# Performance work log

Hardware: AMD Instinct MI355X
Metric: run time of the kernel (lower is better)

The kernel has to match this reference:

```python
import jax, jax.numpy as jnp
import numpy as np

HID = 64      # RNN hidden size (fixed in source)
K = 3         # B-spline order (pykan default)
NUM = 5       # grid intervals (pykan default)
DIMS = [64, 16, 1]  # layer_nums_small_nobi


def make_grid(in_dim):
    # uniform grid on [-1,1] extended by K knots each side -> NUM+2K+1 = 12 knots
    h = 2.0 / NUM
    g = jnp.arange(-K, NUM + K + 1, dtype=jnp.float32) * h - 1.0
    return jnp.broadcast_to(g, (in_dim, g.shape[0]))


def bspline_basis(x, grid):
    # x: (b, in), grid: (in, G) -> basis (b, in, G-K-1) via Cox-de Boor
    xe = x[..., None]
    B = ((xe >= grid[:, :-1]) & (xe < grid[:, 1:])).astype(x.dtype)
    for d in range(1, K + 1):
        left = (xe - grid[:, :-(d + 1)]) / (grid[:, d:-1] - grid[:, :-(d + 1)]) * B[..., :-1]
        right = (grid[:, d + 1:] - xe) / (grid[:, d + 1:] - grid[:, 1:-d]) * B[..., 1:]
        B = left + right
    return B  # (b, in, NUM+K)


def kan_layer(x, grid, coef, sb, sp):
    # coef: (in, out, NUM+K); sb, sp: (in, out)
    bas = bspline_basis(x, grid)                      # (b, in, NUM+K)
    spl = jnp.einsum('bik,iok->bio', bas, coef)       # per-edge spline value
    return jnp.einsum('bi,io->bo', jax.nn.silu(x), sb) + jnp.einsum('bio,io->bo', spl, sp)


def rnn_layer(x, w_ih, w_hh, b_ih, b_hh, return_seq):
    # x: (b, t, f), tanh RNN, h0 = 0
    h0 = jnp.zeros((x.shape[0], HID), x.dtype)
    def step(h, xt):
        h = jnp.tanh(xt @ w_ih.T + h @ w_hh.T + b_ih + b_hh)
        return h, (h if return_seq else 0.0)
    hT, ys = jax.lax.scan(step, h0, jnp.swapaxes(x, 0, 1))
    return jnp.swapaxes(ys, 0, 1) if return_seq else hT


def setup_inputs() -> dict:
    key = jax.random.key(0)
    ks = jax.random.split(key, 16)
    Bsz, T, F = 2048, 256, 64
    s = 1.0 / np.sqrt(HID)
    inp = {'x': jax.random.normal(ks[0], (Bsz, T, F), jnp.float32)}
    inp['w_ih0'] = jax.random.uniform(ks[1], (HID, F), jnp.float32, -s, s)
    inp['w_hh0'] = jax.random.uniform(ks[2], (HID, HID), jnp.float32, -s, s)
    inp['b_ih0'] = jax.random.uniform(ks[3], (HID,), jnp.float32, -s, s)
    inp['b_hh0'] = jax.random.uniform(ks[4], (HID,), jnp.float32, -s, s)
    inp['w_ih1'] = jax.random.uniform(ks[5], (HID, HID), jnp.float32, -s, s)
    inp['w_hh1'] = jax.random.uniform(ks[6], (HID, HID), jnp.float32, -s, s)
    inp['b_ih1'] = jax.random.uniform(ks[7], (HID,), jnp.float32, -s, s)
    inp['b_hh1'] = jax.random.uniform(ks[8], (HID,), jnp.float32, -s, s)
    kk = 9
    for i, (di, do) in enumerate(zip(DIMS[:-1], DIMS[1:])):
        inp[f'grid{i}'] = make_grid(di)
        inp[f'coef{i}'] = 0.1 * jax.random.normal(ks[kk], (di, do, NUM + K), jnp.float32)
        inp[f'sb{i}'] = (1.0 / np.sqrt(di)) * jnp.ones((di, do), jnp.float32) + 0.05 * jax.random.normal(ks[kk + 1], (di, do), jnp.float32)
        inp[f'sp{i}'] = jnp.ones((di, do), jnp.float32)
        kk += 2
    return inp


def reference(x, w_ih0, w_hh0, b_ih0, b_hh0, w_ih1, w_hh1, b_ih1, b_hh1,
              grid0, coef0, sb0, sp0, grid1, coef1, sb1, sp1):
    h1 = rnn_layer(x, w_ih0, w_hh0, b_ih0, b_hh0, return_seq=True)   # (b,t,64)
    out = rnn_layer(h1, w_ih1, w_hh1, b_ih1, b_hh1, return_seq=False)  # last step only
    out = kan_layer(out, grid0, coef0, sb0, sp0)   # (b,16)
    out = kan_layer(out, grid1, coef1, sb1, sp1)   # (b,1)
    return jnp.squeeze(jax.nn.sigmoid(out), 1)     # (b,)
```

## Files before the change

### kernel.cpp

```cpp
#include <hip/hip_runtime.h>
#include <cstdint>
#include <cstddef>

typedef __attribute__((ext_vector_type(8))) __bf16 bf16x8;
typedef __attribute__((ext_vector_type(4))) float f32x4;

#define MFMA16(a, b, c) __builtin_amdgcn_mfma_f32_16x16x32_bf16((a), (b), (c), 0, 0, 0)

__device__ __forceinline__ float fast_tanh(float z) {
    float e = __expf(2.0f * z);
    return 1.0f - 2.0f * __builtin_amdgcn_rcpf(e + 1.0f);
}
__device__ __forceinline__ float fast_sigmoid(float z) {
    return __builtin_amdgcn_rcpf(1.0f + __expf(-z));
}

__device__ __forceinline__ f32x4 gload4(const float* p) {
    return *(const __attribute__((address_space(1))) f32x4*)p;
}

__device__ __forceinline__ unsigned pk2(float a, float b) {
    union { __bf16 h[2]; unsigned u; } p;
    p.h[0] = (__bf16)a;
    p.h[1] = (__bf16)b;
    return p.u;
}

__device__ __forceinline__ bf16x8 cvt8(f32x4 a, f32x4 b) {
    bf16x8 f;
    f[0] = (__bf16)a[0]; f[1] = (__bf16)a[1]; f[2] = (__bf16)a[2]; f[3] = (__bf16)a[3];
    f[4] = (__bf16)b[0]; f[5] = (__bf16)b[1]; f[6] = (__bf16)b[2]; f[7] = (__bf16)b[3];
    return f;
}

__device__ __forceinline__ bf16x8 ldwfrag(const float* __restrict__ W, int row, int k0) {
    const f32x4 a = *(const f32x4*)(W + row * 64 + k0);
    const f32x4 b = *(const f32x4*)(W + row * 64 + k0 + 4);
    return cvt8(a, b);
}

__device__ __forceinline__ void bspl8(float x, const float* kn, float* B) {
    float b[11];
#pragma unroll
    for (int m = 0; m < 11; ++m)
        b[m] = (x >= kn[m] && x < kn[m + 1]) ? 1.0f : 0.0f;
#pragma unroll
    for (int d = 1; d <= 3; ++d) {
#pragma unroll
        for (int m = 0; m + d < 11; ++m) {
            float lf = (x - kn[m]) / (kn[m + d] - kn[m]) * b[m];
            float rt = (kn[m + d + 1] - x) / (kn[m + d + 1] - kn[m + 1]) * b[m + 1];
            b[m] = lf + rt;
        }
    }
#pragma unroll
    for (int m = 0; m < 8; ++m) B[m] = b[m];
}

__global__ __launch_bounds__(256, 1) void rnn_kan_v6(
    const float* __restrict__ x,
    const float* __restrict__ wih0, const float* __restrict__ whh0,
    const float* __restrict__ bih0, const float* __restrict__ bhh0,
    const float* __restrict__ wih1, const float* __restrict__ whh1,
    const float* __restrict__ bih1, const float* __restrict__ bhh1,
    const float* __restrict__ grid0, const float* __restrict__ coef0,
    const float* __restrict__ sb0, const float* __restrict__ sp0,
    const float* __restrict__ grid1, const float* __restrict__ coef1,
    const float* __restrict__ sb1, const float* __restrict__ sp1,
    float* __restrict__ out)
{
    __shared__ __align__(16) unsigned char s_h[2][4096];
    __shared__ __align__(16) float s_hf[16][68];
    __shared__ __align__(16) float s_bas[1024][12];
    __shared__ __align__(16) float s_e[16][17];

    const int tid  = threadIdx.x;
    const int wv   = tid >> 6;
    const int lane = tid & 63;
    const int sc   = lane & 15;
    const int gr   = lane >> 4;
    const int s0   = blockIdx.x << 4;

    const int wrow = 16 * wv + sc;
    const int kofs = 8 * gr;
    bf16x8 fWih0[2], fWhh0[2], fWih1[2], fWhh1[2];
#pragma unroll
    for (int kt = 0; kt < 2; ++kt) {
        fWih0[kt] = ldwfrag(wih0, wrow, 32 * kt + kofs);
        fWhh0[kt] = ldwfrag(whh0, wrow, 32 * kt + kofs);
        fWih1[kt] = ldwfrag(wih1, wrow, 32 * kt + kofs);
        fWhh1[kt] = ldwfrag(whh1, wrow, 32 * kt + kofs);
    }
    f32x4 b0v, b1v, zv;
#pragma unroll
    for (int i = 0; i < 4; ++i) {
        const int h = 16 * wv + 4 * gr + i;
        b0v[i] = bih0[h] + bhh0[h];
        b1v[i] = bih1[h] + bhh1[h];
        zv[i] = 0.0f;
    }

    const unsigned swz  = (unsigned)(sc & 7) << 4;
    const unsigned offW  = sc * 128 + (((unsigned)(32 * wv + 8 * gr)) ^ swz);
    const unsigned offR0 = sc * 128 + (((unsigned)(16 * gr)) ^ swz);
    const unsigned offR1 = sc * 128 + (((unsigned)(64 + 16 * gr)) ^ swz);

    const float* xb = x + (size_t)(s0 + sc) * 16384 + kofs;

    f32x4 q0 = gload4(xb),        q1 = gload4(xb + 4);
    f32x4 q2 = gload4(xb + 32),   q3 = gload4(xb + 36);
    f32x4 p0 = gload4(xb + 64),   p1 = gload4(xb + 68);
    f32x4 p2 = gload4(xb + 96),   p3 = gload4(xb + 100);
    f32x4 r0[3], r1[3], r2[3], r3[3];
#pragma unroll
    for (int j = 0; j < 3; ++j) {
        const float* pj = xb + (size_t)(2 + j) * 64;
        r0[j] = gload4(pj);      r1[j] = gload4(pj + 4);
        r2[j] = gload4(pj + 32); r3[j] = gload4(pj + 36);
    }

    f32x4 xz = MFMA16(fWih0[0], cvt8(q0, q1), b0v);
    xz = MFMA16(fWih0[1], cvt8(q2, q3), xz);

    {
        float v[4];
#pragma unroll
        for (int i = 0; i < 4; ++i) v[i] = fast_tanh(xz[i]);
        uint2 pw; pw.x = pk2(v[0], v[1]); pw.y = pk2(v[2], v[3]);
        *(uint2*)((char*)(&s_h[0][0]) + offW) = pw;
    }
    *(uint2*)((char*)(&s_h[0][0]) + 2048 + offW) = make_uint2(0u, 0u);

    xz = MFMA16(fWih0[0], cvt8(p0, p1), b0v);
    xz = MFMA16(fWih0[1], cvt8(p2, p3), xz);

    asm volatile("s_waitcnt lgkmcnt(0)" ::: "memory");
    __builtin_amdgcn_s_barrier();
    asm volatile("" ::: "memory");

    bf16x8 h1f0 = *(const bf16x8*)((const char*)(&s_h[0][0]) + offR0);
    bf16x8 h1f1 = *(const bf16x8*)((const char*)(&s_h[0][0]) + offR1);
    f32x4 h2z = b1v;

#pragma unroll 3
    for (int t = 1; t < 256; ++t) {
        const int slot = (t - 1) % 3;
        char* hb = (char*)(&s_h[0][0]) + ((t & 1) << 12);

        f32x4 z1a = MFMA16(fWhh0[0], h1f0, xz);
        f32x4 z1b = MFMA16(fWhh0[1], h1f1, zv);
        f32x4 z2a = MFMA16(fWih1[0], h1f0, h2z);
        f32x4 z2b = MFMA16(fWih1[1], h1f1, zv);

        f32x4 z1 = z1a + z1b;
        float v1[4];
#pragma unroll
        for (int i = 0; i < 4; ++i) v1[i] = fast_tanh(z1[i]);
        uint2 pw1; pw1.x = pk2(v1[0], v1[1]); pw1.y = pk2(v1[2], v1[3]);
        *(uint2*)(hb + offW) = pw1;

        f32x4 z2 = z2a + z2b;
        float v2[4];
#pragma unroll
        for (int i = 0; i < 4; ++i) v2[i] = fast_tanh(z2[i]);
        uint2 pw2; pw2.x = pk2(v2[0], v2[1]); pw2.y = pk2(v2[2], v2[3]);
        *(uint2*)(hb + 2048 + offW) = pw2;

        xz = MFMA16(fWih0[0], cvt8(r0[slot], r1[slot]), b0v);
        xz = MFMA16(fWih0[1], cvt8(r2[slot], r3[slot]), xz);
        {
            const float* pn = xb + (size_t)((t + 4 > 255) ? 255 : t + 4) * 64;
            r0[slot] = gload4(pn);      r1[slot] = gload4(pn + 4);
            r2[slot] = gload4(pn + 32); r3[slot] = gload4(pn + 36);
        }

        asm volatile("s_waitcnt lgkmcnt(0)" ::: "memory");
        __builtin_amdgcn_s_barrier();
        asm volatile("" ::: "memory");

        h1f0 = *(const bf16x8*)(hb + offR0);
        h1f1 = *(const bf16x8*)(hb + offR1);
        bf16x8 h2f0 = *(const bf16x8*)(hb + 2048 + offR0);
        bf16x8 h2f1 = *(const bf16x8*)(hb + 2048 + offR1);

        h2z = MFMA16(fWhh1[0], h2f0, b1v);
        h2z = MFMA16(fWhh1[1], h2f1, h2z);
    }

    {
        f32x4 z2a = MFMA16(fWih1[0], h1f0, h2z);
        f32x4 z2b = MFMA16(fWih1[1], h1f1, zv);
        f32x4 z2 = z2a + z2b;
        f32x4 hv;
#pragma unroll
        for (int i = 0; i < 4; ++i) hv[i] = fast_tanh(z2[i]);
        *(f32x4*)(&s_hf[sc][16 * wv + 4 * gr]) = hv;
    }
    __syncthreads();

    float kn0[12], kn1[12];
#pragma unroll
    for (int m = 0; m < 12; ++m) { kn0[m] = grid0[m]; kn1[m] = grid1[m]; }

    for (int q = tid; q < 1024; q += 256) {
        const int i = q >> 4, s = q & 15;
        const float v = s_hf[s][i];
        float B[8];
        bspl8(v, kn0, B);
        *(float4*)(&s_bas[q][0]) = make_float4(B[0], B[1], B[2], B[3]);
        *(float4*)(&s_bas[q][4]) = make_float4(B[4], B[5], B[6], B[7]);
        s_bas[q][8] = v * fast_sigmoid(v);
    }
    __syncthreads();

    {
        const int s = tid >> 4, o = tid & 15;
        float acc = 0.0f;
        for (int i = 0; i < 64; ++i) {
            const int q = (i << 4) + s;
            const float4 B0 = *(const float4*)(&s_bas[q][0]);
            const float4 B1 = *(const float4*)(&s_bas[q][4]);
            const float sil = s_bas[q][8];
            const float* cp = coef0 + i * 128 + o * 8;
            const float4 c0 = *(const float4*)cp;
            const float4 c1 = *(const float4*)(cp + 4);
            const float spl = B0.x * c0.x + B0.y * c0.y + B0.z * c0.z + B0.w * c0.w +
                              B1.x * c1.x + B1.y * c1.y + B1.z * c1.z + B1.w * c1.w;
            acc += sil * sb0[(i << 4) + o] + sp0[(i << 4) + o] * spl;
        }
        float B[8];
        bspl8(acc, kn1, B);
        const float* cp = coef1 + o * 8;
        float spl = 0.0f;
#pragma unroll
        for (int k = 0; k < 8; ++k) spl += B[k] * cp[k];
        s_e[s][o] = (acc * fast_sigmoid(acc)) * sb1[o] + sp1[o] * spl;
    }
    __syncthreads();

    if (tid < 16) {
        float sum = 0.0f;
#pragma unroll
        for (int o = 0; o < 16; ++o) sum += s_e[tid][o];
        out[s0 + tid] = fast_sigmoid(sum);
    }
}

extern "C" void kernel_launch(void* const* d_in, const int* in_sizes, int n_in,
                              void* d_out, int out_size, void* d_ws, size_t ws_size,
                              hipStream_t stream) {
    (void)n_in; (void)out_size; (void)d_ws; (void)ws_size;
    const int B = in_sizes[0] / (256 * 64);
    const int grid = B / 16;
    rnn_kan_v6<<<dim3(grid), dim3(256), 0, stream>>>(
        (const float*)d_in[0],
        (const float*)d_in[1], (const float*)d_in[2], (const float*)d_in[3], (const float*)d_in[4],
        (const float*)d_in[5], (const float*)d_in[6], (const float*)d_in[7], (const float*)d_in[8],
        (const float*)d_in[9], (const float*)d_in[10], (const float*)d_in[11], (const float*)d_in[12],
        (const float*)d_in[13], (const float*)d_in[14], (const float*)d_in[15], (const float*)d_in[16],
        (float*)d_out);
}
```

Before: 146.5 us.

## Split RNN recurrence into three warp-specialized roles pipelined across timesteps

The block grows from 4 to 12 waves, split into three roles. One role computes the input projection for layer 0 and the input-to-hidden product for layer 1, one runs the layer-0 recurrence, and one runs the layer-1 recurrence one step behind, all handing data through double-buffered shared memory. This shortens the serial dependency chain per barrier and spreads the MFMA and tanh work over more waves. In exchange the loop runs two extra steps and needs more shared memory, and the larger block can lower occupancy and make each barrier more expensive.

Result: slower. 358.5 us (+144.7%).

```diff
diff --git a/kernel.cpp b/kernel.cpp
--- a/kernel.cpp
+++ b/kernel.cpp
@@ -57,7 +57,7 @@
     for (int m = 0; m < 8; ++m) B[m] = b[m];
 }
 
-__global__ __launch_bounds__(256, 1) void rnn_kan_v6(
+__global__ __launch_bounds__(768) void rnn_kan_v8(
     const float* __restrict__ x,
     const float* __restrict__ wih0, const float* __restrict__ whh0,
     const float* __restrict__ bih0, const float* __restrict__ bhh0,
@@ -69,7 +69,10 @@
     const float* __restrict__ sb1, const float* __restrict__ sp1,
     float* __restrict__ out)
 {
-    __shared__ __align__(16) unsigned char s_h[2][4096];
+    __shared__ __align__(16) float s_xz[2][16 * 64];
+    __shared__ __align__(16) float s_p2[2][16 * 64];
+    __shared__ __align__(16) unsigned char s_h1[2][2048];
+    __shared__ __align__(16) unsigned char s_h2[2][2048];
     __shared__ __align__(16) float s_hf[16][68];
     __shared__ __align__(16) float s_bas[1024][12];
     __shared__ __align__(16) float s_e[16][17];
@@ -79,130 +82,117 @@
     const int lane = tid & 63;
     const int sc   = lane & 15;
     const int gr   = lane >> 4;
+    const int role = wv >> 2;
+    const int rt   = wv & 3;
     const int s0   = blockIdx.x << 4;
 
-    const int wrow = 16 * wv + sc;
-    const int kofs = 8 * gr;
-    bf16x8 fWih0[2], fWhh0[2], fWih1[2], fWhh1[2];
-#pragma unroll
-    for (int kt = 0; kt < 2; ++kt) {
-        fWih0[kt] = ldwfrag(wih0, wrow, 32 * kt + kofs);
-        fWhh0[kt] = ldwfrag(whh0, wrow, 32 * kt + kofs);
-        fWih1[kt] = ldwfrag(wih1, wrow, 32 * kt + kofs);
-        fWhh1[kt] = ldwfrag(whh1, wrow, 32 * kt + kofs);
-    }
-    f32x4 b0v, b1v, zv;
-#pragma unroll
-    for (int i = 0; i < 4; ++i) {
-        const int h = 16 * wv + 4 * gr + i;
-        b0v[i] = bih0[h] + bhh0[h];
-        b1v[i] = bih1[h] + bhh1[h];
-        zv[i] = 0.0f;
-    }
-
     const unsigned swz  = (unsigned)(sc & 7) << 4;
-    const unsigned offW  = sc * 128 + (((unsigned)(32 * wv + 8 * gr)) ^ swz);
+    const unsigned offW  = sc * 128 + (((unsigned)(32 * rt + 8 * gr)) ^ swz);
     const unsigned offR0 = sc * 128 + (((unsigned)(16 * gr)) ^ swz);
     const unsigned offR1 = sc * 128 + (((unsigned)(64 + 16 * gr)) ^ swz);
-
-    const float* xb = x + (size_t)(s0 + sc) * 16384 + kofs;
-
-    f32x4 q0 = gload4(xb),        q1 = gload4(xb + 4);
-    f32x4 q2 = gload4(xb + 32),   q3 = gload4(xb + 36);
-    f32x4 p0 = gload4(xb + 64),   p1 = gload4(xb + 68);
-    f32x4 p2 = gload4(xb + 96),   p3 = gload4(xb + 100);
-    f32x4 r0[3], r1[3], r2[3], r3[3];
-#pragma unroll
-    for (int j = 0; j < 3; ++j) {
-        const float* pj = xb + (size_t)(2 + j) * 64;
-        r0[j] = gload4(pj);      r1[j] = gload4(pj + 4);
-        r2[j] = gload4(pj + 32); r3[j] = gload4(pj + 36);
-    }
-
-    f32x4 xz = MFMA16(fWih0[0], cvt8(q0, q1), b0v);
-    xz = MFMA16(fWih0[1], cvt8(q2, q3), xz);
-
-    {
-        float v[4];
-#pragma unroll
-        for (int i = 0; i < 4; ++i) v[i] = fast_tanh(xz[i]);
-        uint2 pw; pw.x = pk2(v[0], v[1]); pw.y = pk2(v[2], v[3]);
-        *(uint2*)((char*)(&s_h[0][0]) + offW) = pw;
-    }
-    *(uint2*)((char*)(&s_h[0][0]) + 2048 + offW) = make_uint2(0u, 0u);
-
-    xz = MFMA16(fWih0[0], cvt8(p0, p1), b0v);
-    xz = MFMA16(fWih0[1], cvt8(p2, p3), xz);
-
-    asm volatile("s_waitcnt lgkmcnt(0)" ::: "memory");
-    __builtin_amdgcn_s_barrier();
-    asm volatile("" ::: "memory");
-
-    bf16x8 h1f0 = *(const bf16x8*)((const char*)(&s_h[0][0]) + offR0);
-    bf16x8 h1f1 = *(const bf16x8*)((const char*)(&s_h[0][0]) + offR1);
-    f32x4 h2z = b1v;
-
-#pragma unroll 3
-    for (int t = 1; t < 256; ++t) {
-        const int slot = (t - 1) % 3;
-        char* hb = (char*)(&s_h[0][0]) + ((t & 1) << 12);
-
-        f32x4 z1a = MFMA16(fWhh0[0], h1f0, xz);
-        f32x4 z1b = MFMA16(fWhh0[1], h1f1, zv);
-        f32x4 z2a = MFMA16(fWih1[0], h1f0, h2z);
-        f32x4 z2b = MFMA16(fWih1[1], h1f1, zv);
-
-        f32x4 z1 = z1a + z1b;
-        float v1[4];
-#pragma unroll
-        for (int i = 0; i < 4; ++i) v1[i] = fast_tanh(z1[i]);
-        uint2 pw1; pw1.x = pk2(v1[0], v1[1]); pw1.y = pk2(v1[2], v1[3]);
-        *(uint2*)(hb + offW) = pw1;
-
-        f32x4 z2 = z2a + z2b;
-        float v2[4];
-#pragma unroll
-        for (int i = 0; i < 4; ++i) v2[i] = fast_tanh(z2[i]);
-        uint2 pw2; pw2.x = pk2(v2[0], v2[1]); pw2.y = pk2(v2[2], v2[3]);
-        *(uint2*)(hb + 2048 + offW) = pw2;
-
-        xz = MFMA16(fWih0[0], cvt8(r0[slot], r1[slot]), b0v);
-        xz = MFMA16(fWih0[1], cvt8(r2[slot], r3[slot]), xz);
-        {
-            const float* pn = xb + (size_t)((t + 4 > 255) ? 255 : t + 4) * 64;
-            r0[slot] = gload4(pn);      r1[slot] = gload4(pn + 4);
-            r2[slot] = gload4(pn + 32); r3[slot] = gload4(pn + 36);
-        }
-
+    const unsigned offX  = sc * 256 + (((unsigned)(64 * rt + 16 * gr)) ^ swz);
+
+    for (int i = tid; i < 512; i += 768) ((unsigned*)&s_h1[1][0])[i] = 0u;
+    for (int i = tid; i < 1024; i += 768) ((unsigned*)&s_h2[0][0])[i] = 0u;
+
+    bf16x8 fA0, fA1, fB0, fB1;
+    f32x4 b0a, b1a;
+    const float* xb = x + (size_t)(s0 + sc) * 16384 + 8 * gr;
+    f32x4 r0[2], r1[2], r2[2], r3[2];
+
+    if (role == 0) {
+        fA0 = ldwfrag(wih0, 16 * rt + sc, 8 * gr);
+        fA1 = ldwfrag(wih0, 16 * rt + sc, 32 + 8 * gr);
+        fB0 = ldwfrag(wih1, 16 * rt + sc, 8 * gr);
+        fB1 = ldwfrag(wih1, 16 * rt + sc, 32 + 8 * gr);
+#pragma unroll
+        for (int i = 0; i < 4; ++i) {
+            const int h = 16 * rt + 4 * gr + i;
+            b0a[i] = bih0[h] + bhh0[h];
+            b1a[i] = bih1[h] + bhh1[h];
+        }
+        f32x4 q0 = gload4(xb),      q1 = gload4(xb + 4);
+        f32x4 q2 = gload4(xb + 32), q3 = gload4(xb + 36);
+        r0[1] = gload4(xb + 64);  r1[1] = gload4(xb + 68);
+        r2[1] = gload4(xb + 96);  r3[1] = gload4(xb + 100);
+        r0[0] = gload4(xb + 128); r1[0] = gload4(xb + 132);
+        r2[0] = gload4(xb + 160); r3[0] = gload4(xb + 164);
+        f32x4 a = MFMA16(fA0, cvt8(q0, q1), b0a);
+        a = MFMA16(fA1, cvt8(q2, q3), a);
+        *(f32x4*)((char*)&s_xz[0][0] + offX) = a;
+    } else if (role == 1) {
+        fA0 = ldwfrag(whh0, 16 * rt + sc, 8 * gr);
+        fA1 = ldwfrag(whh0, 16 * rt + sc, 32 + 8 * gr);
+    } else {
+        fA0 = ldwfrag(whh1, 16 * rt + sc, 8 * gr);
+        fA1 = ldwfrag(whh1, 16 * rt + sc, 32 + 8 * gr);
+    }
+    __syncthreads();
+
+    for (int t = 0; t < 258; ++t) {
+        const int par = t & 1;
+        if (role == 0) {
+            if (t < 255) {
+                bf16x8 xf0 = cvt8(r0[par ^ 1], r1[par ^ 1]);
+                bf16x8 xf1 = cvt8(r2[par ^ 1], r3[par ^ 1]);
+                const float* pn = xb + (size_t)((t + 3 > 255) ? 255 : t + 3) * 64;
+                r0[par ^ 1] = gload4(pn);      r1[par ^ 1] = gload4(pn + 4);
+                r2[par ^ 1] = gload4(pn + 32); r3[par ^ 1] = gload4(pn + 36);
+                f32x4 a = MFMA16(fA0, xf0, b0a);
+                a = MFMA16(fA1, xf1, a);
+                *(f32x4*)((char*)&s_xz[par ^ 1][0] + offX) = a;
+            }
+            if (t <= 256) {
+                bf16x8 h1f0 = *(const bf16x8*)((const char*)&s_h1[par ^ 1][0] + offR0);
+                bf16x8 h1f1 = *(const bf16x8*)((const char*)&s_h1[par ^ 1][0] + offR1);
+                f32x4 p = MFMA16(fB0, h1f0, b1a);
+                p = MFMA16(fB1, h1f1, p);
+                *(f32x4*)((char*)&s_p2[par][0] + offX) = p;
+            }
+        } else if (role == 1) {
+            if (t <= 255) {
+                f32x4 xzf = *(const f32x4*)((const char*)&s_xz[par][0] + offX);
+                bf16x8 h1f0 = *(const bf16x8*)((const char*)&s_h1[par ^ 1][0] + offR0);
+                bf16x8 h1f1 = *(const bf16x8*)((const char*)&s_h1[par ^ 1][0] + offR1);
+                f32x4 z = MFMA16(fA0, h1f0, xzf);
+                z = MFMA16(fA1, h1f1, z);
+                float v[4];
+#pragma unroll
+                for (int i = 0; i < 4; ++i) v[i] = fast_tanh(z[i]);
+                uint2 pw; pw.x = pk2(v[0], v[1]); pw.y = pk2(v[2], v[3]);
+                *(uint2*)((char*)&s_h1[par][0] + offW) = pw;
+            }
+        } else {
+            if (t >= 2) {
+                f32x4 p2f = *(const f32x4*)((const char*)&s_p2[par ^ 1][0] + offX);
+                bf16x8 h2f0 = *(const bf16x8*)((const char*)&s_h2[par ^ 1][0] + offR0);
+                bf16x8 h2f1 = *(const bf16x8*)((const char*)&s_h2[par ^ 1][0] + offR1);
+                f32x4 z = MFMA16(fA0, h2f0, p2f);
+                z = MFMA16(fA1, h2f1, z);
+                float v[4];
+#pragma unroll
+                for (int i = 0; i < 4; ++i) v[i] = fast_tanh(z[i]);
+                if (t <= 256) {
+                    uint2 pw; pw.x = pk2(v[0], v[1]); pw.y = pk2(v[2], v[3]);
+                    *(uint2*)((char*)&s_h2[par][0] + offW) = pw;
+                } else {
+                    f32x4 hv;
+#pragma unroll
+                    for (int i = 0; i < 4; ++i) hv[i] = v[i];
+                    *(f32x4*)(&s_hf[sc][16 * rt + 4 * gr]) = hv;
+                }
+            }
+        }
         asm volatile("s_waitcnt lgkmcnt(0)" ::: "memory");
         __builtin_amdgcn_s_barrier();
         asm volatile("" ::: "memory");
-
-        h1f0 = *(const bf16x8*)(hb + offR0);
-        h1f1 = *(const bf16x8*)(hb + offR1);
-        bf16x8 h2f0 = *(const bf16x8*)(hb + 2048 + offR0);
-        bf16x8 h2f1 = *(const bf16x8*)(hb + 2048 + offR1);
-
-        h2z = MFMA16(fWhh1[0], h2f0, b1v);
-        h2z = MFMA16(fWhh1[1], h2f1, h2z);
-    }
-
-    {
-        f32x4 z2a = MFMA16(fWih1[0], h1f0, h2z);
-        f32x4 z2b = MFMA16(fWih1[1], h1f1, zv);
-        f32x4 z2 = z2a + z2b;
-        f32x4 hv;
-#pragma unroll
-        for (int i = 0; i < 4; ++i) hv[i] = fast_tanh(z2[i]);
-        *(f32x4*)(&s_hf[sc][16 * wv + 4 * gr]) = hv;
-    }
-    __syncthreads();
+    }
 
     float kn0[12], kn1[12];
 #pragma unroll
     for (int m = 0; m < 12; ++m) { kn0[m] = grid0[m]; kn1[m] = grid1[m]; }
 
-    for (int q = tid; q < 1024; q += 256) {
+    for (int q = tid; q < 1024; q += 768) {
         const int i = q >> 4, s = q & 15;
         const float v = s_hf[s][i];
         float B[8];
@@ -213,7 +203,7 @@
     }
     __syncthreads();
 
-    {
+    if (tid < 256) {
         const int s = tid >> 4, o = tid & 15;
         float acc = 0.0f;
         for (int i = 0; i < 64; ++i) {
@@ -252,7 +242,7 @@
     (void)n_in; (void)out_size; (void)d_ws; (void)ws_size;
     const int B = in_sizes[0] / (256 * 64);
     const int grid = B / 16;
-    rnn_kan_v6<<<dim3(grid), dim3(256), 0, stream>>>(
+    rnn_kan_v8<<<dim3(grid), dim3(768), 0, stream>>>(
         (const float*)d_in[0],
         (const float*)d_in[1], (const float*)d_in[2], (const float*)d_in[3], (const float*)d_in[4],
         (const float*)d_in[5], (const float*)d_in[6], (const float*)d_in[7], (const float*)d_in[8],
```
